# Kernel optimization log

Measured on AMD Instinct MI355X. Metric: run time of the kernel, lower is better.

## Reference

```python
import jax, jax.numpy as jnp
import numpy as np

N = 50000      # nodes
E = 800000     # edges
HID = 64       # hidden_dim
HEADS = 4
DH = HID // HEADS
PIN = 128      # person_in_dim
DIN = 64       # disease_in_dim
NEXP = 4       # num_experts
K = 2          # topk
L = 2          # n_layers
NEG = 0.2      # gat_neg_slope


def setup_inputs() -> dict:
    key = jax.random.key(0)
    ks = iter(jax.random.split(key, 64))
    nrm = lambda shp, s=0.05: jax.random.normal(next(ks), shp, jnp.float32) * s
    d = {}
    d["features"] = jax.random.normal(next(ks), (N, PIN), jnp.float32)
    d["node_types"] = jax.random.randint(next(ks), (N,), 0, 2)
    d["src"] = jax.random.randint(next(ks), (E,), 0, N)
    d["dst"] = jax.random.randint(next(ks), (E,), 0, N)
    d["W_person"] = nrm((PIN, HID)); d["b_person"] = jnp.zeros((HID,), jnp.float32)
    d["W_disease"] = nrm((DIN, HID)); d["b_disease"] = jnp.zeros((HID,), jnp.float32)
    d["gat_W"] = nrm((L, HID, HID)); d["gat_al"] = nrm((L, HEADS, DH)); d["gat_ar"] = nrm((L, HEADS, DH))
    d["gin_eps"] = jnp.zeros((L,), jnp.float32)
    d["gin_W1"] = nrm((L, HID, HID)); d["gin_b1"] = jnp.zeros((L, HID), jnp.float32)
    d["gin_W2"] = nrm((L, HID, HID)); d["gin_b2"] = jnp.zeros((L, HID), jnp.float32)
    for p in ("gat", "gin"):
        d[p + "_gW"] = nrm((HID, NEXP)); d[p + "_gb"] = jnp.zeros((NEXP,), jnp.float32)
        d[p + "_eW1"] = nrm((NEXP, HID, HID // 2)); d[p + "_eb1"] = jnp.zeros((NEXP, HID // 2), jnp.float32)
        d[p + "_eW2"] = nrm((NEXP, HID // 2, HID)); d[p + "_eb2"] = jnp.zeros((NEXP, HID), jnp.float32)
    d["fg_W1"] = nrm((2 * HID, HID)); d["fg_b1"] = jnp.zeros((HID,), jnp.float32)
    d["fg_W2"] = nrm((HID, HID)); d["fg_b2"] = jnp.zeros((HID,), jnp.float32)
    return d


def _edge_softmax(logits, dst):
    m = jax.ops.segment_max(logits, dst, num_segments=N)
    e = jnp.exp(logits - m[dst])
    s = jax.ops.segment_sum(e, dst, num_segments=N)
    return e / (s[dst] + 1e-9)


def _gat(h, src, dst, gat_W, gat_al, gat_ar):
    for l in range(L):
        hW = (h @ gat_W[l]).reshape(N, HEADS, DH)
        el = (hW * gat_al[l]).sum(-1)                    # [N, HEADS]
        er = (hW * gat_ar[l]).sum(-1)
        lg = jax.nn.leaky_relu(el[src] + er[dst], NEG)   # [E, HEADS]
        a = _edge_softmax(lg, dst)
        out = jax.ops.segment_sum(hW[src] * a[:, :, None], dst, num_segments=N)
        h2 = out.reshape(N, HID) + h                     # residual=True
        h = jax.nn.relu(h2) if l < L - 1 else h2
    return h


def _gin(h, src, dst, gin_eps, gin_W1, gin_b1, gin_W2, gin_b2):
    deg = jax.ops.segment_sum(jnp.ones((E,), jnp.float32), dst, num_segments=N)
    inv = 1.0 / jnp.maximum(deg, 1.0)
    for l in range(L):
        agg = jax.ops.segment_sum(h[src], dst, num_segments=N) * inv[:, None]  # 'mean' aggregator
        x = (1.0 + gin_eps[l]) * h + agg                 # learn_eps=True
        x = jax.nn.relu(x @ gin_W1[l] + gin_b1[l]) @ gin_W2[l] + gin_b2[l]     # 2-layer MLP
        h = jax.nn.relu(x) if l < L - 1 else x
    return h


def _expert(h, gW, gb, eW1, eb1, eW2, eb2):
    probs = jax.nn.softmax(h @ gW + gb, axis=-1)         # [N, NEXP]
    topv, topi = jax.lax.top_k(probs, K)
    topv = topv / topv.sum(-1, keepdims=True)
    hot = jax.nn.one_hot(topi, NEXP, dtype=h.dtype)      # [N, K, NEXP]
    w = (hot * topv[..., None]).sum(1)                   # [N, NEXP] sparse weights
    e1 = jax.nn.relu(jnp.einsum('nd,edh->neh', h, eW1) + eb1)
    e2 = jnp.einsum('neh,ehd->ned', e1, eW2) + eb2       # [N, NEXP, HID]
    out = (e2 * w[:, :, None]).sum(1)
    f = hot.sum(1).mean(0)                               # routed fraction per expert
    P = probs.mean(0)
    aux = NEXP * jnp.sum(f * P)                          # switch-style load balancing
    return out, aux


def reference(features, node_types, src, dst, W_person, b_person, W_disease, b_disease,
              gat_W, gat_al, gat_ar, gin_eps, gin_W1, gin_b1, gin_W2, gin_b2,
              gat_gW, gat_gb, gat_eW1, gat_eb1, gat_eW2, gat_eb2,
              gin_gW, gin_gb, gin_eW1, gin_eb1, gin_eW2, gin_eb2,
              fg_W1, fg_b1, fg_W2, fg_b2):
    # per-type projection + scatter into shared buffer
    hp = features[:, :PIN] @ W_person + b_person
    hd = features[:, :DIN] @ W_disease + b_disease
    h = jnp.where((node_types == 0)[:, None], hp, hd)
    z_gat = _gat(h, src, dst, gat_W, gat_al, gat_ar)
    z_gin = _gin(h, src, dst, gin_eps, gin_W1, gin_b1, gin_W2, gin_b2)
    zg, aux_g = _expert(z_gat, gat_gW, gat_gb, gat_eW1, gat_eb1, gat_eW2, gat_eb2)
    zi, aux_i = _expert(z_gin, gin_gW, gin_gb, gin_eW1, gin_eb1, gin_eW2, gin_eb2)
    z = zi * zg
    u = jnp.concatenate([zg, zi], axis=-1)
    gate = jax.nn.sigmoid(jax.nn.relu(u @ fg_W1 + fg_b1) @ fg_W2 + fg_b2)
    u_prime = gate  # source calls fusion_gate(u) twice -> identical deterministic value
    z = gate * z + (1.0 - gate) * u_prime
    return z, aux_i + aux_g
```

## Files before the change

kernel.cpp:

```cpp
#include <hip/hip_runtime.h>

#define NN 50000
#define EE 800000
#define NEG 0.2f
#define NBLK_SCAN 196
#define NBG 391
#define NBE 196
#define NBKT 98
#define EPB 4096
#define NSEG 196

typedef __attribute__((ext_vector_type(8))) short s8;
typedef __attribute__((ext_vector_type(4))) float f4;

__device__ __forceinline__ float leaky(float x) { return x > 0.f ? x : NEG * x; }
__device__ __forceinline__ unsigned bf16r(float x) {
    unsigned u = __float_as_uint(x);
    return (u + 0x7fffu + ((u >> 16) & 1u)) >> 16;
}
__device__ __forceinline__ float lo16(unsigned p) { return __uint_as_float(p << 16); }
__device__ __forceinline__ float hi16(unsigned p) { return __uint_as_float(p & 0xffff0000u); }

__device__ __forceinline__ s8 a_from_f32(const float* p) {
    float4 u = *reinterpret_cast<const float4*>(p);
// ... 88 lines not shown
    for (int off = 1; off < 256; off <<= 1) {
        int u = (t >= off) ? sm[t - off] : 0;
        __syncthreads();
        sm[t] += u;
        __syncthreads();
    }
    int incl = sm[t];
    if (i < NN) row_start[i] = bpre[blockIdx.x] + incl - v;
    if (i == NN - 1) row_start[NN] = bpre[blockIdx.x] + incl;
}

__global__ __launch_bounds__(256) void k_binB_pre(
        const int* __restrict__ row_start, const int* __restrict__ seg_off,
        const int* __restrict__ seg_cnt, const unsigned* __restrict__ gseg,
        int* __restrict__ csr_src,
        const float* __restrict__ feat, const int* __restrict__ types,
        const float* __restrict__ Wp, const float* __restrict__ bp,
        const float* __restrict__ Wd, const float* __restrict__ bd,
        const float* __restrict__ gW, const float* __restrict__ al,
        const float* __restrict__ ar,
        float* __restrict__ h0f, unsigned* __restrict__ P,
        float* __restrict__ el, float* __restrict__ er) {
    __shared__ unsigned short WpT[64 * 136];
    __shared__ unsigned short WdT[64 * 72];
    __shared__ unsigned short WgT[64 * 72];
    __shared__ unsigned short y0s[4][16 * 72];
    __shared__ int kur[512];
    if (blockIdx.x < NBKT) {
        int b = blockIdx.x;
        int t = threadIdx.x;
        int* spre = (int*)WpT;
        int* soff = (int*)WdT;
        int* ss   = (int*)WgT;
        int c0 = (2 * t     < NSEG) ? seg_cnt[(2 * t)     * NBKT + b] : 0;
        int c1 = (2 * t + 1 < NSEG) ? seg_cnt[(2 * t + 1) * NBKT + b] : 0;
        if (2 * t     < NSEG) soff[2 * t]     = seg_off[(2 * t)     * NBKT + b];
        if (2 * t + 1 < NSEG) soff[2 * t + 1] = seg_off[(2 * t + 1) * NBKT + b];
        ss[t] = c0 + c1;
        __syncthreads();
        for (int off = 1; off < 256; off <<= 1) {
            int u = (t >= off) ? ss[t - off] : 0;
            __syncthreads();
            ss[t] += u;
            __syncthreads();
        }
        int base = ss[t] - (c0 + c1);
        if (2 * t     < NSEG) spre[2 * t]     = base;
        if (2 * t + 1 < NSEG) spre[2 * t + 1] = base + c0;
        if (t == 0) spre[NSEG] = ss[255];
        int d0 = b << 9;
        for (int i = t; i < 512; i += 256) {
            int d = d0 + i;
            kur[i] = (d < NN) ? row_start[d] : 0;
        }
        __syncthreads();
        int cntb = spre[NSEG];
        for (int idx = t; idx < cntb; idx += 256) {
            int lo = 0, hi = NSEG - 1;
            #pragma unroll
            for (int s = 0; s < 8; s++) {
                int mid = (lo + hi + 1) >> 1;
                if (spre[mid] <= idx) lo = mid; else hi = mid - 1;
            }
            unsigned v = gseg[(size_t)lo * EPB + soff[lo] + (idx - spre[lo])];
            int p = atomicAdd(&kur[v & 511], 1);
            csr_src[p] = (int)(v >> 9);
        }
        return;
    }
    for (int idx = threadIdx.x; idx < 128 * 64; idx += 256) {
        int k = idx >> 6, n = idx & 63;
        WpT[n * 136 + k] = (unsigned short)bf16r(Wp[idx]);
    }
    for (int idx = threadIdx.x; idx < 64 * 64; idx += 256) {
        int k = idx >> 6, n = idx & 63;
        WdT[n * 72 + k] = (unsigned short)bf16r(Wd[idx]);
        WgT[n * 72 + k] = (unsigned short)bf16r(gW[idx]);
    }
    __syncthreads();
    int wv = threadIdx.x >> 6, lane = threadIdx.x & 63;
    int quad = lane >> 4, l16 = lane & 15;
    int gw2 = (blockIdx.x - NBKT) * 4 + wv;
    int mtEnd = gw2 * 2 + 2; if (mtEnd > 3125) mtEnd = 3125;
    for (int mt = gw2 * 2; mt < mtEnd; mt++) {
        int row0 = mt * 16;
        const float* arow = feat + (size_t)(row0 + l16) * 128;
        f4 accp[4], accd[4];
        #pragma unroll
        for (int t = 0; t < 4; t++) { accp[t] = f4{0.f,0.f,0.f,0.f}; accd[t] = f4{0.f,0.f,0.f,0.f}; }
        #pragma unroll
        for (int ks = 0; ks < 4; ks++) {
            s8 a = a_from_f32(arow + ks * 32 + quad * 8);
            #pragma unroll
            for (int t = 0; t < 4; t++) {
                s8 b = *(const s8*)&WpT[(t * 16 + l16) * 136 + ks * 32 + quad * 8];
                accp[t] = __builtin_amdgcn_mfma_f32_16x16x32_bf16(a, b, accp[t], 0, 0, 0);
                if (ks < 2) {
                    s8 bd_ = *(const s8*)&WdT[(t * 16 + l16) * 72 + ks * 32 + quad * 8];
                    accd[t] = __builtin_amdgcn_mfma_f32_16x16x32_bf16(a, bd_, accd[t], 0, 0, 0);
                }
            }
        }
        int ty[4];
        #pragma unroll
        for (int r = 0; r < 4; r++) ty[r] = types[row0 + quad * 4 + r];
        float vv[4][4];
        #pragma unroll
        for (int t = 0; t < 4; t++) {
            int col = t * 16 + l16;
            float bpv = bp[col], bdv = bd[col];
            #pragma unroll
            for (int r = 0; r < 4; r++) {
                float v = ty[r] ? (accd[t][r] + bdv) : (accp[t][r] + bpv);
                vv[t][r] = v;
                h0f[(size_t)(row0 + quad * 4 + r) * 64 + col] = v;
                y0s[wv][(quad * 4 + r) * 72 + col] = (unsigned short)bf16r(v);
            }
        }
        s8 a0 = *(const s8*)&y0s[wv][l16 * 72 + quad * 8];
        s8 a1 = *(const s8*)&y0s[wv][l16 * 72 + 32 + quad * 8];
        f4 hw[4];
        #pragma unroll
        for (int t = 0; t < 4; t++) {
            hw[t] = f4{0.f,0.f,0.f,0.f};
            s8 b0 = *(const s8*)&WgT[(t * 16 + l16) * 72 + quad * 8];
            hw[t] = __builtin_amdgcn_mfma_f32_16x16x32_bf16(a0, b0, hw[t], 0, 0, 0);
            s8 b1_ = *(const s8*)&WgT[(t * 16 + l16) * 72 + 32 + quad * 8];
            hw[t] = __builtin_amdgcn_mfma_f32_16x16x32_bf16(a1, b1_, hw[t], 0, 0, 0);
        }
        #pragma unroll
        for (int t = 0; t < 4; t++) {
            int col = t * 16 + l16;
            float alv = al[col], arv = ar[col];
            #pragma unroll
            for (int r = 0; r < 4; r++) {
                int row = row0 + quad * 4 + r;
                float h = hw[t][r];
                P[(size_t)row * 64 + col] = bf16r(h) | (bf16r(vv[t][r]) << 16);
                float pl = h * alv, pr = h * arv;
                #pragma unroll
                for (int m = 1; m < 16; m <<= 1) {
                    pl += __shfl_xor(pl, m, 64);
                    pr += __shfl_xor(pr, m, 64);
                }
                if (l16 == 0) {
                    el[(size_t)row * 4 + t] = pl;
                    er[(size_t)row * 4 + t] = pr;
                }
            }
        }
    }
}

template <int RELU>
__global__ void k_edges(const int* __restrict__ rows, const int* __restrict__ csr,
                        const unsigned* __restrict__ Pin,
                        const float* __restrict__ el, const float* __restrict__ er,
                        const float* __restrict__ gat_in, const float* __restrict__ gin_in,
                        const float* __restrict__ eps_p,
                        float* __restrict__ vgf, unsigned short* __restrict__ vgb,
                        unsigned short* __restrict__ xb) {
    __shared__ float ews[4][256];
    int wv = threadIdx.x >> 6, lane = threadIdx.x & 63;
    int n = blockIdx.x * 4 + wv;
    int st = rows[n], dg = rows[n + 1] - st;
    int hd = lane >> 4;
    float4 erv = *reinterpret_cast<const float4*>(er + (size_t)n * 4);
    float accg = 0.f, acci = 0.f, ssum = 0.f;
    for (int base = 0; base < dg; base += 64) {
        int rem = dg - base; if (rem > 64) rem = 64;
        int myi = 0;
        if (lane < rem) {
            myi = csr[st + base + lane];
            float4 lv = *reinterpret_cast<const float4*>(el + (size_t)myi * 4);
            float4 ev;
            ev.x = __expf(leaky(lv.x + erv.x));
            ev.y = __expf(leaky(lv.y + erv.y));
            ev.z = __expf(leaky(lv.z + erv.z));
            ev.w = __expf(leaky(lv.w + erv.w));
            *reinterpret_cast<float4*>(&ews[wv][lane * 4]) = ev;
        }
        int j = 0;
        for (; j + 4 <= rem; j += 4) {
            int s0 = __shfl(myi, j, 64),     s1 = __shfl(myi, j + 1, 64);
            int s2 = __shfl(myi, j + 2, 64), s3 = __shfl(myi, j + 3, 64);
            unsigned p0 = Pin[(size_t)s0 * 64 + lane];
            unsigned p1 = Pin[(size_t)s1 * 64 + lane];
            unsigned p2 = Pin[(size_t)s2 * 64 + lane];
            unsigned p3 = Pin[(size_t)s3 * 64 + lane];
            float a0 = ews[wv][(j + 0) * 4 + hd];
            float a1 = ews[wv][(j + 1) * 4 + hd];
            float a2 = ews[wv][(j + 2) * 4 + hd];
            float a3 = ews[wv][(j + 3) * 4 + hd];
            accg += a0 * lo16(p0) + a1 * lo16(p1) + a2 * lo16(p2) + a3 * lo16(p3);
            acci += hi16(p0) + hi16(p1) + hi16(p2) + hi16(p3);
            ssum += a0 + a1 + a2 + a3;
        }
        for (; j < rem; j++) {
            int s0 = __shfl(myi, j, 64);
            unsigned p0 = Pin[(size_t)s0 * 64 + lane];
            float a0 = ews[wv][j * 4 + hd];
            accg += a0 * lo16(p0); acci += hi16(p0); ssum += a0;
        }
    }
    float vg = accg / (ssum + 1e-9f) + gat_in[(size_t)n * 64 + lane];
    if (RELU) vg = fmaxf(vg, 0.f);
    float invd = 1.0f / fmaxf((float)dg, 1.0f);
    float x = (1.0f + eps_p[0]) * gin_in[(size_t)n * 64 + lane] + acci * invd;
    size_t off = (size_t)n * 64 + lane;
    vgf[off] = vg;
    vgb[off] = (unsigned short)bf16r(vg);
    xb[off] = (unsigned short)bf16r(x);
}

template <int L>
__global__ __launch_bounds__(256) void k_mlp(const unsigned short* __restrict__ Gx,
        const unsigned short* __restrict__ Eb,
        const float* __restrict__ W1, const float* __restrict__ b1,
        const float* __restrict__ W2, const float* __restrict__ b2,
        const float* __restrict__ gatW, const float* __restrict__ al,
        const float* __restrict__ ar,
        unsigned short* __restrict__ Fb, float* __restrict__ Cf,
        unsigned* __restrict__ P, float* __restrict__ el, float* __restrict__ er,
        const float* __restrict__ Zg, const float* __restrict__ ggW,
        const float* __restrict__ ggb, const float* __restrict__ igW,
        const float* __restrict__ igb,
        float* __restrict__ wgtg, float* __restrict__ wgti,
        float* __restrict__ stats) {
    __shared__ unsigned short W1T[64 * 72];
    __shared__ unsigned short W2T[64 * 72];
    __shared__ unsigned short WgT[(L == 0) ? 64 * 72 : 64];
    __shared__ unsigned short y1s[4][16 * 72];
    __shared__ float sstat[16];
    if (L == 1 && threadIdx.x < 16) sstat[threadIdx.x] = 0.f;
    for (int idx = threadIdx.x; idx < 64 * 64; idx += 256) {
        int k = idx >> 6, n = idx & 63;
        W1T[n * 72 + k] = (unsigned short)bf16r(W1[idx]);
        W2T[n * 72 + k] = (unsigned short)bf16r(W2[idx]);
        if (L == 0) WgT[n * 72 + k] = (unsigned short)bf16r(gatW[idx]);
    }
    __syncthreads();
    int wv = threadIdx.x >> 6, lane = threadIdx.x & 63;
    int quad = lane >> 4, l16 = lane & 15;
    int gw = blockIdx.x * 4 + wv;
    int mtEnd = gw * 2 + 2; if (mtEnd > 3125) mtEnd = 3125;
    float sp[2][4] = {{0,0,0,0},{0,0,0,0}};
    float sh[2][4] = {{0,0,0,0},{0,0,0,0}};
    for (int mt = gw * 2; mt < mtEnd; mt++) {
        int row0 = mt * 16;
        const unsigned short* arow = Gx + (size_t)(row0 + l16) * 64;
        s8 a0 = *(const s8*)(arow + quad * 8);
        s8 a1 = *(const s8*)(arow + 32 + quad * 8);
        f4 acc1[4];
        #pragma unroll
        for (int t = 0; t < 4; t++) {
            acc1[t] = f4{0.f,0.f,0.f,0.f};
            s8 b0 = *(const s8*)&W1T[(t * 16 + l16) * 72 + quad * 8];
            acc1[t] = __builtin_amdgcn_mfma_f32_16x16x32_bf16(a0, b0, acc1[t], 0, 0, 0);
            s8 b1_ = *(const s8*)&W1T[(t * 16 + l16) * 72 + 32 + quad * 8];
            acc1[t] = __builtin_amdgcn_mfma_f32_16x16x32_bf16(a1, b1_, acc1[t], 0, 0, 0);
        }
        #pragma unroll
        for (int t = 0; t < 4; t++) {
            float b1v = b1[t * 16 + l16];
            #pragma unroll
            for (int r = 0; r < 4; r++) {
                float v = fmaxf(acc1[t][r] + b1v, 0.f);
                y1s[wv][(quad * 4 + r) * 72 + t * 16 + l16] = (unsigned short)bf16r(v);
            }
        }
        s8 c0 = *(const s8*)&y1s[wv][l16 * 72 + quad * 8];
        s8 c1 = *(const s8*)&y1s[wv][l16 * 72 + 32 + quad * 8];
        f4 acc2[4];
        #pragma unroll
        for (int t = 0; t < 4; t++) {
            acc2[t] = f4{0.f,0.f,0.f,0.f};
            s8 b0 = *(const s8*)&W2T[(t * 16 + l16) * 72 + quad * 8];
            acc2[t] = __builtin_amdgcn_mfma_f32_16x16x32_bf16(c0, b0, acc2[t], 0, 0, 0);
            s8 b1_ = *(const s8*)&W2T[(t * 16 + l16) * 72 + 32 + quad * 8];
            acc2[t] = __builtin_amdgcn_mfma_f32_16x16x32_bf16(c1, b1_, acc2[t], 0, 0, 0);
        }
        unsigned short vb[4][4];
        float vout[4][4];
        #pragma unroll
        for (int t = 0; t < 4; t++) {
            int col = t * 16 + l16;
            float b2v = b2[col];
            #pragma unroll
            for (int r = 0; r < 4; r++) {
                float v = acc2[t][r] + b2v;
                if (L == 0) v = fmaxf(v, 0.f);
                size_t off = (size_t)(row0 + quad * 4 + r) * 64 + col;
                unsigned short vb16 = (unsigned short)bf16r(v);
                vb[t][r] = vb16;
                vout[t][r] = v;
                Fb[off] = vb16;
                if (L == 0) Cf[off] = v;
            }
        }
        if (L == 0) {
            const unsigned short* erow = Eb + (size_t)(row0 + l16) * 64;
            s8 e0 = *(const s8*)(erow + quad * 8);
            s8 e1 = *(const s8*)(erow + 32 + quad * 8);
            f4 hw[4];
            #pragma unroll
            for (int t = 0; t < 4; t++) {
                hw[t] = f4{0.f,0.f,0.f,0.f};
                s8 b0 = *(const s8*)&WgT[(t * 16 + l16) * 72 + quad * 8];
                hw[t] = __builtin_amdgcn_mfma_f32_16x16x32_bf16(e0, b0, hw[t], 0, 0, 0);
                s8 b1_ = *(const s8*)&WgT[(t * 16 + l16) * 72 + 32 + quad * 8];
                hw[t] = __builtin_amdgcn_mfma_f32_16x16x32_bf16(e1, b1_, hw[t], 0, 0, 0);
            }
            #pragma unroll
            for (int t = 0; t < 4; t++) {
                int col = t * 16 + l16;
                float alv = al[col], arv = ar[col];
                #pragma unroll
                for (int r = 0; r < 4; r++) {
                    int row = row0 + quad * 4 + r;
                    float h = hw[t][r];
                    P[(size_t)row * 64 + col] = bf16r(h) | ((unsigned)vb[t][r] << 16);
                    float pl = h * alv, pr = h * arv;
                    #pragma unroll
                    for (int m = 1; m < 16; m <<= 1) {
                        pl += __shfl_xor(pl, m, 64);
                        pr += __shfl_xor(pr, m, 64);
                    }
                    if (l16 == 0) {
                        el[(size_t)row * 4 + t] = pl;
                        er[(size_t)row * 4 + t] = pr;
                    }
                }
            }
        } else {
            #pragma unroll
            for (int r = 0; r < 4; r++) {
                int row = row0 + quad * 4 + r;
                float pg[4] = {0,0,0,0}, pi[4] = {0,0,0,0};
                #pragma unroll
                for (int t = 0; t < 4; t++) {
                    int col = t * 16 + l16;
                    float zgv = Zg[(size_t)row * 64 + col];
                    float ziv = vout[t][r];
                    #pragma unroll
                    for (int e = 0; e < 4; e++) {
                        pg[e] += zgv * ggW[col * 4 + e];
                        pi[e] += ziv * igW[col * 4 + e];
                    }
                }
                #pragma unroll
                for (int m = 1; m < 16; m <<= 1) {
                    #pragma unroll
                    for (int e = 0; e < 4; e++) {
                        pg[e] += __shfl_xor(pg[e], m, 64);
                        pi[e] += __shfl_xor(pi[e], m, 64);
                    }
                }
                if (l16 == 0) {
                    #pragma unroll
                    for (int q = 0; q < 2; q++) {
                        float lg0 = (q ? pi[0] + igb[0] : pg[0] + ggb[0]);
                        float lg1 = (q ? pi[1] + igb[1] : pg[1] + ggb[1]);
                        float lg2 = (q ? pi[2] + igb[2] : pg[2] + ggb[2]);
                        float lg3 = (q ? pi[3] + igb[3] : pg[3] + ggb[3]);
                        float mx = fmaxf(fmaxf(lg0, lg1), fmaxf(lg2, lg3));
                        float ex0 = __expf(lg0 - mx), ex1 = __expf(lg1 - mx);
                        float ex2 = __expf(lg2 - mx), ex3 = __expf(lg3 - mx);
                        float inv = 1.0f / (ex0 + ex1 + ex2 + ex3);
                        float pr4[4] = {ex0 * inv, ex1 * inv, ex2 * inv, ex3 * inv};
                        int i1 = 0; float v1 = pr4[0];
                        #pragma unroll
                        for (int t = 1; t < 4; t++) if (pr4[t] > v1) { v1 = pr4[t]; i1 = t; }
                        int i2 = -1; float v2 = -1.f;
                        #pragma unroll
                        for (int t = 0; t < 4; t++) if (t != i1 && pr4[t] > v2) { v2 = pr4[t]; i2 = t; }
                        float wsum = v1 + v2;
                        float wq[4] = {0.f, 0.f, 0.f, 0.f};
                        wq[i1] = v1 / wsum; wq[i2] = v2 / wsum;
                        float* WD = q ? wgti : wgtg;
                        *reinterpret_cast<float4*>(WD + (size_t)row * 4) =
                            float4{wq[0], wq[1], wq[2], wq[3]};
                        #pragma unroll
                        for (int t = 0; t < 4; t++) sp[q][t] += pr4[t];
                        sh[q][i1] += 1.f; sh[q][i2] += 1.f;
                    }
                }
            }
        }
    }
    if (L == 1) {
        __syncthreads();
        if (l16 == 0) {
            #pragma unroll
            for (int q = 0; q < 2; q++)
                #pragma unroll
                for (int e = 0; e < 4; e++) {
                    atomicAdd(&sstat[q * 8 + e], sp[q][e]);
                    atomicAdd(&sstat[q * 8 + 4 + e], sh[q][e]);
                }
        }
        __syncthreads();
        if (threadIdx.x < 16) atomicAdd(&stats[threadIdx.x], sstat[threadIdx.x]);
    }
}

__global__ __launch_bounds__(256) void k_expert(const unsigned short* __restrict__ Eb,
        const unsigned short* __restrict__ Fb,
        const float* __restrict__ g_eW1, const float* __restrict__ g_eb1,
        const float* __restrict__ g_eW2, const float* __restrict__ g_eb2,
        const float* __restrict__ i_eW1, const float* __restrict__ i_eb1,
        const float* __restrict__ i_eW2, const float* __restrict__ i_eb2,
        const float* __restrict__ wgtg, const float* __restrict__ wgti,
        float* __restrict__ moegf, float* __restrict__ moeif,
        unsigned short* __restrict__ ub) {
    __shared__ unsigned short w1t[4 * 32 * 72];
    __shared__ unsigned short w2t[4 * 64 * 40];
    __shared__ unsigned short y1s[4][16 * 40];
    int p = (blockIdx.x >= NBE) ? 1 : 0;
    int bb = blockIdx.x - p * NBE;
    const unsigned short* Ab = p ? Fb : Eb;
    const float* eW1 = p ? i_eW1 : g_eW1;
    const float* eb1 = p ? i_eb1 : g_eb1;
    const float* eW2 = p ? i_eW2 : g_eW2;
    const float* eb2 = p ? i_eb2 : g_eb2;
    const float* wgt = p ? wgti : wgtg;
    float* moef = p ? moeif : moegf;
    int qoff = p ? 64 : 0;
    for (int g = threadIdx.x; g < 8192; g += 256) {
        int e = g >> 11, rem = g & 2047;
        int k = rem >> 5, n = rem & 31;
        w1t[e * 2304 + n * 72 + k] = (unsigned short)bf16r(eW1[g]);
    }
    for (int g = threadIdx.x; g < 8192; g += 256) {
        int e = g >> 11, rem = g & 2047;
        int k = rem >> 6, n = rem & 63;
        w2t[e * 2560 + n * 40 + k] = (unsigned short)bf16r(eW2[g]);
    }
    __syncthreads();
    int wv = threadIdx.x >> 6, lane = threadIdx.x & 63;
    int quad = lane >> 4, l16 = lane & 15;
    int gw = bb * 4 + wv;
    int mtEnd = gw * 4 + 4; if (mtEnd > 3125) mtEnd = 3125;
    for (int mt = gw * 4; mt < mtEnd; mt++) {
        int row0 = mt * 16;
        const unsigned short* arow = Ab + (size_t)(row0 + l16) * 64;
        s8 a0 = *(const s8*)(arow + quad * 8);
        s8 a1 = *(const s8*)(arow + 32 + quad * 8);
        f4 outacc[4];
        #pragma unroll
        for (int t = 0; t < 4; t++) outacc[t] = f4{0.f,0.f,0.f,0.f};
        for (int e = 0; e < 4; e++) {
            f4 acc1[2];
            #pragma unroll
            for (int t = 0; t < 2; t++) {
                acc1[t] = f4{0.f,0.f,0.f,0.f};
                s8 b0 = *(const s8*)&w1t[e * 2304 + (t * 16 + l16) * 72 + quad * 8];
                acc1[t] = __builtin_amdgcn_mfma_f32_16x16x32_bf16(a0, b0, acc1[t], 0, 0, 0);
                s8 b1_ = *(const s8*)&w1t[e * 2304 + (t * 16 + l16) * 72 + 32 + quad * 8];
                acc1[t] = __builtin_amdgcn_mfma_f32_16x16x32_bf16(a1, b1_, acc1[t], 0, 0, 0);
            }
            #pragma unroll
            for (int t = 0; t < 2; t++) {
                float b1v = eb1[e * 32 + t * 16 + l16];
                #pragma unroll
                for (int r = 0; r < 4; r++) {
                    float v = fmaxf(acc1[t][r] + b1v, 0.f);
                    y1s[wv][(quad * 4 + r) * 40 + t * 16 + l16] = (unsigned short)bf16r(v);
                }
            }
            s8 a2 = *(const s8*)&y1s[wv][l16 * 40 + quad * 8];
            f4 acc2[4];
            #pragma unroll
            for (int t = 0; t < 4; t++) {
                acc2[t] = f4{0.f,0.f,0.f,0.f};
                s8 b2_ = *(const s8*)&w2t[e * 2560 + (t * 16 + l16) * 40 + quad * 8];
                acc2[t] = __builtin_amdgcn_mfma_f32_16x16x32_bf16(a2, b2_, acc2[t], 0, 0, 0);
            }
            #pragma unroll
            for (int t = 0; t < 4; t++) {
                float b2v = eb2[e * 64 + t * 16 + l16];
                #pragma unroll
                for (int r = 0; r < 4; r++) {
                    float we = wgt[(size_t)(row0 + quad * 4 + r) * 4 + e];
                    outacc[t][r] += we * (acc2[t][r] + b2v);
                }
            }
        }
        #pragma unroll
        for (int t = 0; t < 4; t++) {
            int col = t * 16 + l16;
            #pragma unroll
            for (int r = 0; r < 4; r++) {
                int row = row0 + quad * 4 + r;
                float v = outacc[t][r];
                moef[(size_t)row * 64 + col] = v;
                ub[(size_t)row * 128 + qoff + col] = (unsigned short)bf16r(v);
            }
        }
    }
}

__global__ __launch_bounds__(256) void k_fusion(const unsigned short* __restrict__ ubuf,
        const float* __restrict__ W1, const float* __restrict__ b1,
        const float* __restrict__ W2, const float* __restrict__ b2,
        const float* __restrict__ moegf, const float* __restrict__ moeif,
        float* __restrict__ out, const float* __restrict__ stats) {
    __shared__ unsigned short W1T[64 * 136];
    __shared__ unsigned short W2T[64 * 72];
    __shared__ unsigned short y1s[4][16 * 72];
    for (int idx = threadIdx.x; idx < 128 * 64; idx += 256) {
        int k = idx >> 6, n = idx & 63;
        W1T[n * 136 + k] = (unsigned short)bf16r(W1[idx]);
    }
    for (int idx = threadIdx.x; idx < 64 * 64; idx += 256) {
        int k = idx >> 6, n = idx & 63;
        W2T[n * 72 + k] = (unsigned short)bf16r(W2[idx]);
    }
    __syncthreads();
    int wv = threadIdx.x >> 6, lane = threadIdx.x & 63;
    int quad = lane >> 4, l16 = lane & 15;
    int gw = blockIdx.x * 4 + wv;
    int mtEnd = gw * 2 + 2; if (mtEnd > 3125) mtEnd = 3125;
    for (int mt = gw * 2; mt < mtEnd; mt++) {
        int row0 = mt * 16;
        const unsigned short* arow = ubuf + (size_t)(row0 + l16) * 128;
        f4 acc1[4];
        #pragma unroll
        for (int t = 0; t < 4; t++) acc1[t] = f4{0.f,0.f,0.f,0.f};
        #pragma unroll
        for (int ks = 0; ks < 4; ks++) {
            s8 a = *(const s8*)(arow + ks * 32 + quad * 8);
            #pragma unroll
            for (int t = 0; t < 4; t++) {
                s8 b = *(const s8*)&W1T[(t * 16 + l16) * 136 + ks * 32 + quad * 8];
                acc1[t] = __builtin_amdgcn_mfma_f32_16x16x32_bf16(a, b, acc1[t], 0, 0, 0);
            }
        }
        #pragma unroll
        for (int t = 0; t < 4; t++) {
            float b1v = b1[t * 16 + l16];
            #pragma unroll
            for (int r = 0; r < 4; r++) {
                float v = fmaxf(acc1[t][r] + b1v, 0.f);
                y1s[wv][(quad * 4 + r) * 72 + t * 16 + l16] = (unsigned short)bf16r(v);
            }
        }
        f4 acc2[4];
        #pragma unroll
        for (int t = 0; t < 4; t++) acc2[t] = f4{0.f,0.f,0.f,0.f};
        #pragma unroll
        for (int ks = 0; ks < 2; ks++) {
            s8 a = *(const s8*)&y1s[wv][l16 * 72 + ks * 32 + quad * 8];
            #pragma unroll
            for (int t = 0; t < 4; t++) {
                s8 b = *(const s8*)&W2T[(t * 16 + l16) * 72 + ks * 32 + quad * 8];
                acc2[t] = __builtin_amdgcn_mfma_f32_16x16x32_bf16(a, b, acc2[t], 0, 0, 0);
            }
        }
        #pragma unroll
        for (int t = 0; t < 4; t++) {
            int col = t * 16 + l16;
            float b2v = b2[col];
            #pragma unroll
            for (int r = 0; r < 4; r++) {
                int row = row0 + quad * 4 + r;
                float g = 1.0f / (1.0f + __expf(-(acc2[t][r] + b2v)));
                float zgv = moegf[(size_t)row * 64 + col];
                float ziv = moeif[(size_t)row * 64 + col];
                out[(size_t)row * 64 + col] = g * zgv * ziv + (1.0f - g) * g;
            }
        }
    }
    if (blockIdx.x == 0 && threadIdx.x < 64) {
        int t = threadIdx.x;
        float s = (t < 16) ? stats[t] : 0.f;
        float aux = 0.f;
        for (int q = 0; q < 2; q++) {
            float a = 0.f;
            for (int e = 0; e < 4; e++) {
                float pr = __shfl(s, q * 8 + e, 64);
                float f  = __shfl(s, q * 8 + 4 + e, 64);
                a += (f / (float)NN) * (pr / (float)NN);
            }
            aux += 4.0f * a;
        }
        if (t == 0) out[(size_t)NN * 64] = aux;
    }
}

extern "C" void kernel_launch(void* const* d_in, const int* in_sizes, int n_in,
                              void* d_out, int out_size, void* d_ws, size_t ws_size,
                              hipStream_t stream) {
    (void)in_sizes; (void)n_in; (void)out_size; (void)ws_size;
    const float* features  = (const float*)d_in[0];
    const int*   node_types= (const int*)d_in[1];
    const int*   src       = (const int*)d_in[2];
    const int*   dst       = (const int*)d_in[3];
    const float* W_person  = (const float*)d_in[4];
    const float* b_person  = (const float*)d_in[5];
    const float* W_disease = (const float*)d_in[6];
    const float* b_disease = (const float*)d_in[7];
    const float* gat_W     = (const float*)d_in[8];
    const float* gat_al    = (const float*)d_in[9];
    const float* gat_ar    = (const float*)d_in[10];
    const float* gin_eps   = (const float*)d_in[11];
    const float* gin_W1    = (const float*)d_in[12];
    const float* gin_b1    = (const float*)d_in[13];
    const float* gin_W2    = (const float*)d_in[14];
    const float* gin_b2    = (const float*)d_in[15];
    const float* gat_gW    = (const float*)d_in[16];
    const float* gat_gb    = (const float*)d_in[17];
    const float* gat_eW1   = (const float*)d_in[18];
    const float* gat_eb1   = (const float*)d_in[19];
    const float* gat_eW2   = (const float*)d_in[20];
    const float* gat_eb2   = (const float*)d_in[21];
    const float* gin_gW    = (const float*)d_in[22];
    const float* gin_gb    = (const float*)d_in[23];
    const float* gin_eW1   = (const float*)d_in[24];
    const float* gin_eb1   = (const float*)d_in[25];
    const float* gin_eW2   = (const float*)d_in[26];
    const float* gin_eb2   = (const float*)d_in[27];
    const float* fg_W1     = (const float*)d_in[28];
    const float* fg_b1     = (const float*)d_in[29];
    const float* fg_W2     = (const float*)d_in[30];
    const float* fg_b2     = (const float*)d_in[31];
    float* out = (float*)d_out;

    float* ws = (float*)d_ws;
    size_t o = 0;
    float* A = ws + o; o += (size_t)NN * 64;
    float* B = ws + o; o += (size_t)NN * 64;
    float* C = ws + o; o += (size_t)NN * 64;
    unsigned short* E  = (unsigned short*)(ws + o); o += (size_t)NN * 32;
    unsigned short* F  = (unsigned short*)(ws + o); o += (size_t)NN * 32;
    unsigned short* G  = (unsigned short*)(ws + o); o += (size_t)NN * 32;
    unsigned* P = (unsigned*)(ws + o); o += (size_t)NN * 64;
    float* el = ws + o; o += (size_t)NN * 4;
    float* er = ws + o; o += (size_t)NN * 4;
    float* wgtg = ws + o; o += (size_t)NN * 4;
    float* wgti = ws + o; o += (size_t)NN * 4;
    int* degcnt    = (int*)(ws + o); o += NN;
    float* stats   = ws + o; o += 16;
    int* row_start = (int*)(ws + o); o += NN + 4;
    int* bsums     = (int*)(ws + o); o += 256;
    int* bpre      = (int*)(ws + o); o += 256;
    int* csr_src   = (int*)(ws + o); o += EE;
    int* seg_off   = (int*)(ws + o); o += NSEG * NBKT + 64;
    int* seg_cnt   = (int*)(ws + o); o += NSEG * NBKT + 64;
    unsigned* gseg = (unsigned*)(ws + o); o += (size_t)NSEG * EPB;

    unsigned short* ub = (unsigned short*)A;

    const int NB_node = NN / 4;

    hipMemsetAsync(degcnt, 0, sizeof(int) * NN + sizeof(float) * 16, stream);

    k_binA<<<NSEG, 256, 0, stream>>>(src, dst, degcnt, seg_off, seg_cnt, gseg);
    k_scan_a<<<NBLK_SCAN, 256, 0, stream>>>(degcnt, bsums);
    k_scan_b<<<1, 256, 0, stream>>>(bsums, bpre);
    k_scan_c<<<NBLK_SCAN, 256, 0, stream>>>(degcnt, bpre, row_start);

    k_binB_pre<<<NBKT + NBG, 256, 0, stream>>>(row_start, seg_off, seg_cnt, gseg, csr_src,
                                               features, node_types, W_person, b_person,
                                               W_disease, b_disease, gat_W, gat_al, gat_ar,
                                               A, P, el, er);

    k_edges<1><<<NB_node, 256, 0, stream>>>(row_start, csr_src, P, el, er, A, A,
                                            gin_eps, B, E, G);
    k_mlp<0><<<NBG, 256, 0, stream>>>(G, E, gin_W1, gin_b1, gin_W2, gin_b2,
                                      gat_W + 4096, gat_al + 64, gat_ar + 64,
                                      F, C, P, el, er,
                                      nullptr, nullptr, nullptr, nullptr, nullptr,
                                      nullptr, nullptr, nullptr);

    k_edges<0><<<NB_node, 256, 0, stream>>>(row_start, csr_src, P, el, er, B, C,
                                            gin_eps + 1, B, E, G);
    k_mlp<1><<<NBG, 256, 0, stream>>>(G, nullptr, gin_W1 + 4096, gin_b1 + 64,
                                      gin_W2 + 4096, gin_b2 + 64,
                                      nullptr, nullptr, nullptr,
                                      F, nullptr, nullptr, nullptr, nullptr,
                                      B, gat_gW, gat_gb, gin_gW, gin_gb,
                                      wgtg, wgti, stats);

    k_expert<<<NBE * 2, 256, 0, stream>>>(E, F,
                                          gat_eW1, gat_eb1, gat_eW2, gat_eb2,
                                          gin_eW1, gin_eb1, gin_eW2, gin_eb2,
                                          wgtg, wgti, B, C, ub);

    k_fusion<<<NBG, 256, 0, stream>>>(ub, fg_W1, fg_b1, fg_W2, fg_b2, B, C, out, stats);
}
```

Baseline: 352.8 us.

## Fuse edge aggregation and per-layer MLP into one 16-node block kernel

```diff
diff --git a/kernel.cpp b/kernel.cpp
--- a/kernel.cpp
+++ b/kernel.cpp
@@ -264,255 +264,226 @@
     }
 }
 
-template <int RELU>
-__global__ void k_edges(const int* __restrict__ rows, const int* __restrict__ csr,
-                        const unsigned* __restrict__ Pin,
-                        const float* __restrict__ el, const float* __restrict__ er,
-                        const float* __restrict__ gat_in, const float* __restrict__ gin_in,
-                        const float* __restrict__ eps_p,
-                        float* __restrict__ vgf, unsigned short* __restrict__ vgb,
-                        unsigned short* __restrict__ xb) {
-    __shared__ float ews[4][256];
-    int wv = threadIdx.x >> 6, lane = threadIdx.x & 63;
-    int n = blockIdx.x * 4 + wv;
-    int st = rows[n], dg = rows[n + 1] - st;
-    int hd = lane >> 4;
-    float4 erv = *reinterpret_cast<const float4*>(er + (size_t)n * 4);
-    float accg = 0.f, acci = 0.f, ssum = 0.f;
-    for (int base = 0; base < dg; base += 64) {
-        int rem = dg - base; if (rem > 64) rem = 64;
-        int myi = 0;
-        if (lane < rem) {
-            myi = csr[st + base + lane];
-            float4 lv = *reinterpret_cast<const float4*>(el + (size_t)myi * 4);
-            float4 ev;
-            ev.x = __expf(leaky(lv.x + erv.x));
-            ev.y = __expf(leaky(lv.y + erv.y));
-            ev.z = __expf(leaky(lv.z + erv.z));
-            ev.w = __expf(leaky(lv.w + erv.w));
-            *reinterpret_cast<float4*>(&ews[wv][lane * 4]) = ev;
-        }
-        int j = 0;
-        for (; j + 4 <= rem; j += 4) {
-            int s0 = __shfl(myi, j, 64),     s1 = __shfl(myi, j + 1, 64);
-            int s2 = __shfl(myi, j + 2, 64), s3 = __shfl(myi, j + 3, 64);
-            unsigned p0 = Pin[(size_t)s0 * 64 + lane];
-            unsigned p1 = Pin[(size_t)s1 * 64 + lane];
-            unsigned p2 = Pin[(size_t)s2 * 64 + lane];
-            unsigned p3 = Pin[(size_t)s3 * 64 + lane];
-            float a0 = ews[wv][(j + 0) * 4 + hd];
-            float a1 = ews[wv][(j + 1) * 4 + hd];
-            float a2 = ews[wv][(j + 2) * 4 + hd];
-            float a3 = ews[wv][(j + 3) * 4 + hd];
-            accg += a0 * lo16(p0) + a1 * lo16(p1) + a2 * lo16(p2) + a3 * lo16(p3);
-            acci += hi16(p0) + hi16(p1) + hi16(p2) + hi16(p3);
-            ssum += a0 + a1 + a2 + a3;
-        }
-        for (; j < rem; j++) {
-            int s0 = __shfl(myi, j, 64);
-            unsigned p0 = Pin[(size_t)s0 * 64 + lane];
-            float a0 = ews[wv][j * 4 + hd];
-            accg += a0 * lo16(p0); acci += hi16(p0); ssum += a0;
-        }
-    }
-    float vg = accg / (ssum + 1e-9f) + gat_in[(size_t)n * 64 + lane];
-    if (RELU) vg = fmaxf(vg, 0.f);
-    float invd = 1.0f / fmaxf((float)dg, 1.0f);
-    float x = (1.0f + eps_p[0]) * gin_in[(size_t)n * 64 + lane] + acci * invd;
-    size_t off = (size_t)n * 64 + lane;
-    vgf[off] = vg;
-    vgb[off] = (unsigned short)bf16r(vg);
-    xb[off] = (unsigned short)bf16r(x);
-}
-
 template <int L>
-__global__ __launch_bounds__(256) void k_mlp(const unsigned short* __restrict__ Gx,
-        const unsigned short* __restrict__ Eb,
+__global__ __launch_bounds__(1024, 8) void k_layer(
+        const int* __restrict__ rows, const int* __restrict__ csr,
+        const unsigned* __restrict__ Pin,
+        const float* __restrict__ el_in, const float* __restrict__ er_in,
+        const float* __restrict__ gat_in, const float* __restrict__ gin_in,
+        const float* __restrict__ eps_p,
         const float* __restrict__ W1, const float* __restrict__ b1,
         const float* __restrict__ W2, const float* __restrict__ b2,
         const float* __restrict__ gatW, const float* __restrict__ al,
         const float* __restrict__ ar,
+        float* __restrict__ vgf_out,
+        unsigned short* __restrict__ Eb_out,
         unsigned short* __restrict__ Fb, float* __restrict__ Cf,
-        unsigned* __restrict__ P, float* __restrict__ el, float* __restrict__ er,
-        const float* __restrict__ Zg, const float* __restrict__ ggW,
-        const float* __restrict__ ggb, const float* __restrict__ igW,
-        const float* __restrict__ igb,
+        unsigned* __restrict__ Pout, float* __restrict__ el_out,
+        float* __restrict__ er_out,
+        const float* __restrict__ ggW, const float* __restrict__ ggb,
+        const float* __restrict__ igW, const float* __restrict__ igb,
         float* __restrict__ wgtg, float* __restrict__ wgti,
         float* __restrict__ stats) {
+    __shared__ float ews[16][256];
     __shared__ unsigned short W1T[64 * 72];
     __shared__ unsigned short W2T[64 * 72];
     __shared__ unsigned short WgT[(L == 0) ? 64 * 72 : 64];
-    __shared__ unsigned short y1s[4][16 * 72];
+    __shared__ unsigned short xs[16 * 72];
+    __shared__ unsigned short vgs[(L == 0) ? 16 * 72 : 64];
+    __shared__ unsigned short y1s[16 * 72];
+    __shared__ unsigned short y2b[(L == 0) ? 16 * 72 : 64];
+    __shared__ float vgf32[(L == 1) ? 16 * 68 : 4];
+    __shared__ float y2f[(L == 1) ? 16 * 68 : 4];
     __shared__ float sstat[16];
-    if (L == 1 && threadIdx.x < 16) sstat[threadIdx.x] = 0.f;
-    for (int idx = threadIdx.x; idx < 64 * 64; idx += 256) {
-        int k = idx >> 6, n = idx & 63;
-        W1T[n * 72 + k] = (unsigned short)bf16r(W1[idx]);
-        W2T[n * 72 + k] = (unsigned short)bf16r(W2[idx]);
-        if (L == 0) WgT[n * 72 + k] = (unsigned short)bf16r(gatW[idx]);
-    }
-    __syncthreads();
-    int wv = threadIdx.x >> 6, lane = threadIdx.x & 63;
+    int tid = threadIdx.x;
+    if (L == 1 && tid < 16) sstat[tid] = 0.f;
+    for (int idx = tid; idx < 64 * 64; idx += 1024) {
+        int k = idx >> 6, nn = idx & 63;
+        W1T[nn * 72 + k] = (unsigned short)bf16r(W1[idx]);
+        W2T[nn * 72 + k] = (unsigned short)bf16r(W2[idx]);
+        if (L == 0) WgT[nn * 72 + k] = (unsigned short)bf16r(gatW[idx]);
+    }
+    int wv = tid >> 6, lane = tid & 63;
+    int n = blockIdx.x * 16 + wv;
+    {
+        int st = rows[n], dg = rows[n + 1] - st;
+        int hd = lane >> 4;
+        float4 erv = *reinterpret_cast<const float4*>(er_in + (size_t)n * 4);
+        float accg = 0.f, acci = 0.f, ssum = 0.f;
+        for (int base = 0; base < dg; base += 64) {
+            int rem = dg - base; if (rem > 64) rem = 64;
+            int myi = 0;
+            if (lane < rem) {
+                myi = csr[st + base + lane];
+                float4 lv = *reinterpret_cast<const float4*>(el_in + (size_t)myi * 4);
+                float4 ev;
+                ev.x = __expf(leaky(lv.x + erv.x));
+                ev.y = __expf(leaky(lv.y + erv.y));
+                ev.z = __expf(leaky(lv.z + erv.z));
+                ev.w = __expf(leaky(lv.w + erv.w));
+                *reinterpret_cast<float4*>(&ews[wv][lane * 4]) = ev;
+            }
+            int j = 0;
+            for (; j + 4 <= rem; j += 4) {
+                int s0 = __shfl(myi, j, 64),     s1 = __shfl(myi, j + 1, 64);
+                int s2 = __shfl(myi, j + 2, 64), s3 = __shfl(myi, j + 3, 64);
+                unsigned p0 = Pin[(size_t)s0 * 64 + lane];
+                unsigned p1 = Pin[(size_t)s1 * 64 + lane];
+                unsigned p2 = Pin[(size_t)s2 * 64 + lane];
+                unsigned p3 = Pin[(size_t)s3 * 64 + lane];
+                float a0 = ews[wv][(j + 0) * 4 + hd];
+                float a1 = ews[wv][(j + 1) * 4 + hd];
+                float a2 = ews[wv][(j + 2) * 4 + hd];
+                float a3 = ews[wv][(j + 3) * 4 + hd];
+                accg += a0 * lo16(p0) + a1 * lo16(p1) + a2 * lo16(p2) + a3 * lo16(p3);
+                acci += hi16(p0) + hi16(p1) + hi16(p2) + hi16(p3);
+                ssum += a0 + a1 + a2 + a3;
+            }
+            for (; j < rem; j++) {
+                int s0 = __shfl(myi, j, 64);
+                unsigned p0 = Pin[(size_t)s0 * 64 + lane];
+                float a0 = ews[wv][j * 4 + hd];
+                accg += a0 * lo16(p0); acci += hi16(p0); ssum += a0;
+            }
+        }
+        float vg = accg / (ssum + 1e-9f) + gat_in[(size_t)n * 64 + lane];
+        if (L == 0) vg = fmaxf(vg, 0.f);
+        float invd = 1.0f / fmaxf((float)dg, 1.0f);
+        float x = (1.0f + eps_p[0]) * gin_in[(size_t)n * 64 + lane] + acci * invd;
+        xs[wv * 72 + lane] = (unsigned short)bf16r(x);
+        if (L == 0) {
+            vgs[wv * 72 + lane] = (unsigned short)bf16r(vg);
+            vgf_out[(size_t)n * 64 + lane] = vg;
+        } else {
+            vgf32[wv * 68 + lane] = vg;
+            Eb_out[(size_t)n * 64 + lane] = (unsigned short)bf16r(vg);
+        }
+    }
+    __syncthreads();
     int quad = lane >> 4, l16 = lane & 15;
-    int gw = blockIdx.x * 4 + wv;
-    int mtEnd = gw * 2 + 2; if (mtEnd > 3125) mtEnd = 3125;
-    float sp[2][4] = {{0,0,0,0},{0,0,0,0}};
-    float sh[2][4] = {{0,0,0,0},{0,0,0,0}};
-    for (int mt = gw * 2; mt < mtEnd; mt++) {
-        int row0 = mt * 16;
-        const unsigned short* arow = Gx + (size_t)(row0 + l16) * 64;
-        s8 a0 = *(const s8*)(arow + quad * 8);
-        s8 a1 = *(const s8*)(arow + 32 + quad * 8);
-        f4 acc1[4];
-        #pragma unroll
-        for (int t = 0; t < 4; t++) {
-            acc1[t] = f4{0.f,0.f,0.f,0.f};
-            s8 b0 = *(const s8*)&W1T[(t * 16 + l16) * 72 + quad * 8];
-            acc1[t] = __builtin_amdgcn_mfma_f32_16x16x32_bf16(a0, b0, acc1[t], 0, 0, 0);
-            s8 b1_ = *(const s8*)&W1T[(t * 16 + l16) * 72 + 32 + quad * 8];
-            acc1[t] = __builtin_amdgcn_mfma_f32_16x16x32_bf16(a1, b1_, acc1[t], 0, 0, 0);
-        }
-        #pragma unroll
-        for (int t = 0; t < 4; t++) {
-            float b1v = b1[t * 16 + l16];
-            #pragma unroll
-            for (int r = 0; r < 4; r++) {
-                float v = fmaxf(acc1[t][r] + b1v, 0.f);
-                y1s[wv][(quad * 4 + r) * 72 + t * 16 + l16] = (unsigned short)bf16r(v);
-            }
-        }
-        s8 c0 = *(const s8*)&y1s[wv][l16 * 72 + quad * 8];
-        s8 c1 = *(const s8*)&y1s[wv][l16 * 72 + 32 + quad * 8];
-        f4 acc2[4];
-        #pragma unroll
-        for (int t = 0; t < 4; t++) {
-            acc2[t] = f4{0.f,0.f,0.f,0.f};
-            s8 b0 = *(const s8*)&W2T[(t * 16 + l16) * 72 + quad * 8];
-            acc2[t] = __builtin_amdgcn_mfma_f32_16x16x32_bf16(c0, b0, acc2[t], 0, 0, 0);
-            s8 b1_ = *(const s8*)&W2T[(t * 16 + l16) * 72 + 32 + quad * 8];
-            acc2[t] = __builtin_amdgcn_mfma_f32_16x16x32_bf16(c1, b1_, acc2[t], 0, 0, 0);
-        }
-        unsigned short vb[4][4];
-        float vout[4][4];
-        #pragma unroll
-        for (int t = 0; t < 4; t++) {
-            int col = t * 16 + l16;
-            float b2v = b2[col];
-            #pragma unroll
-            for (int r = 0; r < 4; r++) {
-                float v = acc2[t][r] + b2v;
-                if (L == 0) v = fmaxf(v, 0.f);
-                size_t off = (size_t)(row0 + quad * 4 + r) * 64 + col;
-                unsigned short vb16 = (unsigned short)bf16r(v);
-                vb[t][r] = vb16;
-                vout[t][r] = v;
-                Fb[off] = vb16;
-                if (L == 0) Cf[off] = v;
-            }
-        }
-        if (L == 0) {
-            const unsigned short* erow = Eb + (size_t)(row0 + l16) * 64;
-            s8 e0 = *(const s8*)(erow + quad * 8);
-            s8 e1 = *(const s8*)(erow + 32 + quad * 8);
-            f4 hw[4];
-            #pragma unroll
-            for (int t = 0; t < 4; t++) {
-                hw[t] = f4{0.f,0.f,0.f,0.f};
-                s8 b0 = *(const s8*)&WgT[(t * 16 + l16) * 72 + quad * 8];
-                hw[t] = __builtin_amdgcn_mfma_f32_16x16x32_bf16(e0, b0, hw[t], 0, 0, 0);
-                s8 b1_ = *(const s8*)&WgT[(t * 16 + l16) * 72 + 32 + quad * 8];
-                hw[t] = __builtin_amdgcn_mfma_f32_16x16x32_bf16(e1, b1_, hw[t], 0, 0, 0);
-            }
-            #pragma unroll
-            for (int t = 0; t < 4; t++) {
-                int col = t * 16 + l16;
-                float alv = al[col], arv = ar[col];
-                #pragma unroll
-                for (int r = 0; r < 4; r++) {
-                    int row = row0 + quad * 4 + r;
-                    float h = hw[t][r];
-                    P[(size_t)row * 64 + col] = bf16r(h) | ((unsigned)vb[t][r] << 16);
-                    float pl = h * alv, pr = h * arv;
-                    #pragma unroll
-                    for (int m = 1; m < 16; m <<= 1) {
-                        pl += __shfl_xor(pl, m, 64);
-                        pr += __shfl_xor(pr, m, 64);
-                    }
-                    if (l16 == 0) {
-                        el[(size_t)row * 4 + t] = pl;
-                        er[(size_t)row * 4 + t] = pr;
-                    }
-                }
-            }
-        } else {
+    int row0 = blockIdx.x * 16;
+    f4 hw = f4{0.f, 0.f, 0.f, 0.f};
+    if (wv < 4) {
+        int t = wv;
+        s8 a0 = *(const s8*)&xs[l16 * 72 + quad * 8];
+        s8 a1 = *(const s8*)&xs[l16 * 72 + 32 + quad * 8];
+        f4 acc1 = f4{0.f, 0.f, 0.f, 0.f};
+        s8 b0 = *(const s8*)&W1T[(t * 16 + l16) * 72 + quad * 8];
+        acc1 = __builtin_amdgcn_mfma_f32_16x16x32_bf16(a0, b0, acc1, 0, 0, 0);
+        s8 b1_ = *(const s8*)&W1T[(t * 16 + l16) * 72 + 32 + quad * 8];
+        acc1 = __builtin_amdgcn_mfma_f32_16x16x32_bf16(a1, b1_, acc1, 0, 0, 0);
+        float b1v = b1[t * 16 + l16];
+        #pragma unroll
+        for (int r = 0; r < 4; r++) {
+            float v = fmaxf(acc1[r] + b1v, 0.f);
+            y1s[(quad * 4 + r) * 72 + t * 16 + l16] = (unsigned short)bf16r(v);
+        }
+    } else if (L == 0 && wv < 8) {
+        int t = wv - 4;
+        s8 e0 = *(const s8*)&vgs[l16 * 72 + quad * 8];
+        s8 e1 = *(const s8*)&vgs[l16 * 72 + 32 + quad * 8];
+        s8 b0 = *(const s8*)&WgT[(t * 16 + l16) * 72 + quad * 8];
+        hw = __builtin_amdgcn_mfma_f32_16x16x32_bf16(e0, b0, hw, 0, 0, 0);
+        s8 b1_ = *(const s8*)&WgT[(t * 16 + l16) * 72 + 32 + quad * 8];
+        hw = __builtin_amdgcn_mfma_f32_16x16x32_bf16(e1, b1_, hw, 0, 0, 0);
+        int col = t * 16 + l16;
+        float alv = al[col], arv = ar[col];
+        #pragma unroll
+        for (int r = 0; r < 4; r++) {
+            float h = hw[r];
+            float pl = h * alv, pr = h * arv;
+            #pragma unroll
+            for (int m = 1; m < 16; m <<= 1) {
+                pl += __shfl_xor(pl, m, 64);
+                pr += __shfl_xor(pr, m, 64);
+            }
+            if (l16 == 0) {
+                int row = row0 + quad * 4 + r;
+                el_out[(size_t)row * 4 + t] = pl;
+                er_out[(size_t)row * 4 + t] = pr;
+            }
+        }
+    }
+    __syncthreads();
+    if (wv < 4) {
+        int t = wv;
+        s8 c0 = *(const s8*)&y1s[l16 * 72 + quad * 8];
+        s8 c1 = *(const s8*)&y1s[l16 * 72 + 32 + quad * 8];
+        f4 acc2 = f4{0.f, 0.f, 0.f, 0.f};
+        s8 b0 = *(const s8*)&W2T[(t * 16 + l16) * 72 + quad * 8];
+        acc2 = __builtin_amdgcn_mfma_f32_16x16x32_bf16(c0, b0, acc2, 0, 0, 0);
+        s8 b1_ = *(const s8*)&W2T[(t * 16 + l16) * 72 + 32 + quad * 8];
+        acc2 = __builtin_amdgcn_mfma_f32_16x16x32_bf16(c1, b1_, acc2, 0, 0, 0);
+        int col = t * 16 + l16;
+        float b2v = b2[col];
+        #pragma unroll
+        for (int r = 0; r < 4; r++) {
+            float v = acc2[r] + b2v;
+            if (L == 0) v = fmaxf(v, 0.f);
+            size_t off = (size_t)(row0 + quad * 4 + r) * 64 + col;
+            if (L == 0) {
+                Cf[off] = v;
+                y2b[(quad * 4 + r) * 72 + col] = (unsigned short)bf16r(v);
+            } else {
+                Fb[off] = (unsigned short)bf16r(v);
+                y2f[(quad * 4 + r) * 68 + col] = v;
+            }
+        }
+    }
+    __syncthreads();
+    if (L == 0) {
+        if (wv >= 4 && wv < 8) {
+            int t = wv - 4, col = t * 16 + l16;
             #pragma unroll
             for (int r = 0; r < 4; r++) {
                 int row = row0 + quad * 4 + r;
-                float pg[4] = {0,0,0,0}, pi[4] = {0,0,0,0};
-                #pragma unroll
-                for (int t = 0; t < 4; t++) {
-                    int col = t * 16 + l16;
-                    float zgv = Zg[(size_t)row * 64 + col];
-                    float ziv = vout[t][r];
+                Pout[(size_t)row * 64 + col] =
+                    bf16r(hw[r]) | ((unsigned)y2b[(quad * 4 + r) * 72 + col] << 16);
+            }
+        }
+    } else {
+        if (wv == 8) {
+            int node = lane >> 2, e = lane & 3;
+            #pragma unroll
+            for (int q = 0; q < 2; q++) {
+                const float* zs = q ? y2f : vgf32;
+                const float* GW = q ? igW : ggW;
+                const float* GB = q ? igb : ggb;
+                float lg = GB[e];
+                #pragma unroll 8
+                for (int k = 0; k < 64; k++) lg += zs[node * 68 + k] * GW[k * 4 + e];
+                float bv = __shfl_xor(lg, 1, 64);
+                float cv = __shfl_xor(lg, 2, 64);
+                float dv = __shfl_xor(bv, 2, 64);
+                float arr[4];
+                arr[e] = lg; arr[e ^ 1] = bv; arr[e ^ 2] = cv; arr[e ^ 3] = dv;
+                if (e == 0) {
+                    float mx = fmaxf(fmaxf(arr[0], arr[1]), fmaxf(arr[2], arr[3]));
+                    float ex0 = __expf(arr[0] - mx), ex1 = __expf(arr[1] - mx);
+                    float ex2 = __expf(arr[2] - mx), ex3 = __expf(arr[3] - mx);
+                    float inv = 1.0f / (ex0 + ex1 + ex2 + ex3);
+                    float pr4[4] = {ex0 * inv, ex1 * inv, ex2 * inv, ex3 * inv};
+                    int i1 = 0; float v1 = pr4[0];
                     #pragma unroll
-                    for (int e = 0; e < 4; e++) {
-                        pg[e] += zgv * ggW[col * 4 + e];
-                        pi[e] += ziv * igW[col * 4 + e];
-                    }
+                    for (int t = 1; t < 4; t++) if (pr4[t] > v1) { v1 = pr4[t]; i1 = t; }
+                    int i2 = -1; float v2 = -1.f;
+                    #pragma unroll
+                    for (int t = 0; t < 4; t++) if (t != i1 && pr4[t] > v2) { v2 = pr4[t]; i2 = t; }
+                    float wsum = v1 + v2;
+                    float wq[4] = {0.f, 0.f, 0.f, 0.f};
+                    wq[i1] = v1 / wsum; wq[i2] = v2 / wsum;
+                    float* WD = q ? wgti : wgtg;
+                    *reinterpret_cast<float4*>(WD + (size_t)(row0 + node) * 4) =
+                        float4{wq[0], wq[1], wq[2], wq[3]};
+                    #pragma unroll
+                    for (int t = 0; t < 4; t++) atomicAdd(&sstat[q * 8 + t], pr4[t]);
+                    atomicAdd(&sstat[q * 8 + 4 + i1], 1.f);
+                    atomicAdd(&sstat[q * 8 + 4 + i2], 1.f);
                 }
-                #pragma unroll
-                for (int m = 1; m < 16; m <<= 1) {
-                    #pragma unroll
-                    for (int e = 0; e < 4; e++) {
-                        pg[e] += __shfl_xor(pg[e], m, 64);
-                        pi[e] += __shfl_xor(pi[e], m, 64);
-                    }
-                }
-                if (l16 == 0) {
-                    #pragma unroll
-                    for (int q = 0; q < 2; q++) {
-                        float lg0 = (q ? pi[0] + igb[0] : pg[0] + ggb[0]);
-                        float lg1 = (q ? pi[1] + igb[1] : pg[1] + ggb[1]);
-                        float lg2 = (q ? pi[2] + igb[2] : pg[2] + ggb[2]);
-                        float lg3 = (q ? pi[3] + igb[3] : pg[3] + ggb[3]);
-                        float mx = fmaxf(fmaxf(lg0, lg1), fmaxf(lg2, lg3));
-                        float ex0 = __expf(lg0 - mx), ex1 = __expf(lg1 - mx);
-                        float ex2 = __expf(lg2 - mx), ex3 = __expf(lg3 - mx);
-                        float inv = 1.0f / (ex0 + ex1 + ex2 + ex3);
-                        float pr4[4] = {ex0 * inv, ex1 * inv, ex2 * inv, ex3 * inv};
-                        int i1 = 0; float v1 = pr4[0];
-                        #pragma unroll
-                        for (int t = 1; t < 4; t++) if (pr4[t] > v1) { v1 = pr4[t]; i1 = t; }
-                        int i2 = -1; float v2 = -1.f;
-                        #pragma unroll
-                        for (int t = 0; t < 4; t++) if (t != i1 && pr4[t] > v2) { v2 = pr4[t]; i2 = t; }
-                        float wsum = v1 + v2;
-                        float wq[4] = {0.f, 0.f, 0.f, 0.f};
-                        wq[i1] = v1 / wsum; wq[i2] = v2 / wsum;
-                        float* WD = q ? wgti : wgtg;
-                        *reinterpret_cast<float4*>(WD + (size_t)row * 4) =
-                            float4{wq[0], wq[1], wq[2], wq[3]};
-                        #pragma unroll
-                        for (int t = 0; t < 4; t++) sp[q][t] += pr4[t];
-                        sh[q][i1] += 1.f; sh[q][i2] += 1.f;
-                    }
-                }
-            }
-        }
-    }
-    if (L == 1) {
-        __syncthreads();
-        if (l16 == 0) {
-            #pragma unroll
-            for (int q = 0; q < 2; q++)
-                #pragma unroll
-                for (int e = 0; e < 4; e++) {
-                    atomicAdd(&sstat[q * 8 + e], sp[q][e]);
-                    atomicAdd(&sstat[q * 8 + 4 + e], sh[q][e]);
-                }
-        }
-        __syncthreads();
-        if (threadIdx.x < 16) atomicAdd(&stats[threadIdx.x], sstat[threadIdx.x]);
+            }
+        }
+        __syncthreads();
+        if (tid < 16) atomicAdd(&stats[tid], sstat[tid]);
     }
 }
 
@@ -745,10 +716,12 @@
     float* C = ws + o; o += (size_t)NN * 64;
     unsigned short* E  = (unsigned short*)(ws + o); o += (size_t)NN * 32;
     unsigned short* F  = (unsigned short*)(ws + o); o += (size_t)NN * 32;
-    unsigned short* G  = (unsigned short*)(ws + o); o += (size_t)NN * 32;
-    unsigned* P = (unsigned*)(ws + o); o += (size_t)NN * 64;
-    float* el = ws + o; o += (size_t)NN * 4;
-    float* er = ws + o; o += (size_t)NN * 4;
+    unsigned* P0 = (unsigned*)(ws + o); o += (size_t)NN * 64;
+    unsigned* P1 = (unsigned*)(ws + o); o += (size_t)NN * 64;
+    float* el0 = ws + o; o += (size_t)NN * 4;
+    float* er0 = ws + o; o += (size_t)NN * 4;
+    float* el1 = ws + o; o += (size_t)NN * 4;
+    float* er1 = ws + o; o += (size_t)NN * 4;
     float* wgtg = ws + o; o += (size_t)NN * 4;
     float* wgti = ws + o; o += (size_t)NN * 4;
     int* degcnt    = (int*)(ws + o); o += NN;
@@ -763,8 +736,6 @@
 
     unsigned short* ub = (unsigned short*)A;
 
-    const int NB_node = NN / 4;
-
     hipMemsetAsync(degcnt, 0, sizeof(int) * NN + sizeof(float) * 16, stream);
 
     k_binA<<<NSEG, 256, 0, stream>>>(src, dst, degcnt, seg_off, seg_cnt, gseg);
@@ -775,24 +746,22 @@
     k_binB_pre<<<NBKT + NBG, 256, 0, stream>>>(row_start, seg_off, seg_cnt, gseg, csr_src,
                                                features, node_types, W_person, b_person,
                                                W_disease, b_disease, gat_W, gat_al, gat_ar,
-                                               A, P, el, er);
-
-    k_edges<1><<<NB_node, 256, 0, stream>>>(row_start, csr_src, P, el, er, A, A,
-                                            gin_eps, B, E, G);
-    k_mlp<0><<<NBG, 256, 0, stream>>>(G, E, gin_W1, gin_b1, gin_W2, gin_b2,
-                                      gat_W + 4096, gat_al + 64, gat_ar + 64,
-                                      F, C, P, el, er,
-                                      nullptr, nullptr, nullptr, nullptr, nullptr,
-                                      nullptr, nullptr, nullptr);
-
-    k_edges<0><<<NB_node, 256, 0, stream>>>(row_start, csr_src, P, el, er, B, C,
-                                            gin_eps + 1, B, E, G);
-    k_mlp<1><<<NBG, 256, 0, stream>>>(G, nullptr, gin_W1 + 4096, gin_b1 + 64,
-                                      gin_W2 + 4096, gin_b2 + 64,
-                                      nullptr, nullptr, nullptr,
-                                      F, nullptr, nullptr, nullptr, nullptr,
-                                      B, gat_gW, gat_gb, gin_gW, gin_gb,
-                                      wgtg, wgti, stats);
+                                               A, P0, el0, er0);
+
+    k_layer<0><<<3125, 1024, 0, stream>>>(row_start, csr_src, P0, el0, er0, A, A, gin_eps,
+                                          gin_W1, gin_b1, gin_W2, gin_b2,
+                                          gat_W + 4096, gat_al + 64, gat_ar + 64,
+                                          B, nullptr, nullptr, C, P1, el1, er1,
+                                          nullptr, nullptr, nullptr, nullptr,
+                                          nullptr, nullptr, nullptr);
+
+    k_layer<1><<<3125, 1024, 0, stream>>>(row_start, csr_src, P1, el1, er1, B, C,
+                                          gin_eps + 1, gin_W1 + 4096, gin_b1 + 64,
+                                          gin_W2 + 4096, gin_b2 + 64,
+                                          nullptr, nullptr, nullptr,
+                                          nullptr, E, F, nullptr, nullptr, nullptr, nullptr,
+                                          gat_gW, gat_gb, gin_gW, gin_gb,
+                                          wgtg, wgti, stats);
 
     k_expert<<<NBE * 2, 256, 0, stream>>>(E, F,
                                           gat_eW1, gat_eb1, gat_eW2, gat_eb2,
```

Result: slower. 410.7 us (+16.4%).
